# Kernel tuning notes

Measured on AMD Instinct MI355X. Metric: run time of the kernel, lower is better.

The kernel has to match this reference:

```python
import jax, jax.numpy as jnp
import numpy as np
import math

B, CK, CV, O, T, H, W = 2, 64, 512, 2, 16, 30, 54


def setup_inputs() -> dict:
    key = jax.random.key(0)
    k1, k2, k3, k4, k5 = jax.random.split(key, 5)
    return {
        'query_key': jax.random.normal(k1, (B, CK, H, W), jnp.float32),
        'query_selection': jax.random.uniform(k2, (B, CK, H, W), jnp.float32),
        'memory_key': jax.random.normal(k3, (B, CK, T, H, W), jnp.float32),
        'memory_shrinkage': jax.random.uniform(k4, (B, 1, T, H, W), jnp.float32),
        'memory_value': jax.random.normal(k5, (B, O, CV, T, H, W), jnp.float32),
    }


def reference(query_key, query_selection, memory_key, memory_shrinkage, memory_value):
    b, ck, h, w = query_key.shape
    t = memory_key.shape[2]
    n = t * h * w          # memory bank size
    hw = h * w             # query size
    o, cv = memory_value.shape[1], memory_value.shape[2]

    mk = memory_key.reshape(b, ck, n)             # B CK N
    ms = memory_shrinkage.reshape(b, 1, n)        # B 1 N
    qk = query_key.reshape(b, ck, hw)             # B CK HW
    qe = query_selection.reshape(b, ck, hw)       # B CK HW

    # negative squared L2 distance, selection-weighted per channel:
    # -sum_c qe_c * (mk_c - qk_c)^2 = -a_sq + 2ab - b_sq
    a_sq = jnp.einsum('bcn,bcq->bnq', mk * mk, qe)          # B N HW
    two_ab = 2.0 * jnp.einsum('bcn,bcq->bnq', mk, qk * qe)  # B N HW
    b_sq = jnp.sum(qe * qk * qk, axis=1, keepdims=True)     # B 1 HW
    similarity = (-a_sq + two_ab - b_sq)
    # shrinkage scaling + 1/sqrt(CK)
    similarity = similarity * ms.reshape(b, n, 1) * (1.0 / math.sqrt(ck))

    # softmax over the memory axis N
    affinity = jax.nn.softmax(similarity, axis=1)           # B N HW

    # weighted readout
    mv = memory_value.reshape(b, o * cv, n)                 # B (O*CV) N
    mem = jnp.einsum('bvn,bnq->bvq', mv, affinity)          # B (O*CV) HW
    return mem.reshape(b, o, cv, h, w)
```

## Files before the change

kernel.cpp:

```cpp
#include <hip/hip_runtime.h>
#include <stdint.h>

#define CKP 128
#define OCV 1024
#define NTOT 25920
#define HW 1620
#define HWP 1664
#define QT 128
#define VT 256
#define NC 64
#define NQT 13
#define NS 2
#define CHUNKS_TOTAL 405
#define CHUNK_SPLIT 203

typedef _Float16 f16x8 __attribute__((ext_vector_type(8)));
typedef _Float16 f16x4 __attribute__((ext_vector_type(4)));
typedef float f32x4 __attribute__((ext_vector_type(4)));

__device__ __forceinline__ void gload_lds16(const void* g, void* l) {
  __builtin_amdgcn_global_load_lds(
      (const __attribute__((address_space(1))) uint32_t*)g,
      (__attribute__((address_space(3))) uint32_t*)l, 16, 0, 0);
}

__global__ void k_prep_mv(const float* __restrict__ mv, _Float16* __restrict__ mvh) {
  int i = blockIdx.x * 256 + threadIdx.x;
  const float4* s = (const float4*)mv + (size_t)i * 2;
  float4 a = s[0], b = s[1];
  f16x8 o;
  o[0]=(_Float16)a.x; o[1]=(_Float16)a.y; o[2]=(_Float16)a.z; o[3]=(_Float16)a.w;
  o[4]=(_Float16)b.x; o[5]=(_Float16)b.y; o[6]=(_Float16)b.z; o[7]=(_Float16)b.w;
  *((f16x8*)mvh + i) = o;
}

__global__ void k_prep_mk(const float* __restrict__ mk, _Float16* __restrict__ mkp) {
  __shared__ _Float16 LT[64 * CKP];
  int b = blockIdx.y, n0 = blockIdx.x * 64;
  int c4 = threadIdx.x >> 6, nl = threadIdx.x & 63;
  for (int c = c4; c < 64; c += 4) {
    float v = mk[((size_t)(b * 64 + c)) * NTOT + n0 + nl];
    LT[nl * CKP + c]      = (_Float16)v;
    LT[nl * CKP + 64 + c] = (_Float16)(v * v);
  }
  __syncthreads();
  #pragma unroll
  for (int k = 0; k < 4; ++k) {
    int idx = threadIdx.x + 256 * k;
    int n = idx >> 4, c16 = idx & 15;
    *((uint4*)(mkp + ((size_t)b * NTOT + n0 + n) * CKP + c16 * 8)) =
        *((const uint4*)(&LT[n * CKP + c16 * 8]));
  }
}

__global__ void k_prep_q(const float* __restrict__ qk, const float* __restrict__ qe,
                         _Float16* __restrict__ qp, float* __restrict__ bsq) {
  __shared__ _Float16 LT[QT * CKP];
  int b = blockIdx.y, q0 = blockIdx.x * QT;
  int t = threadIdx.x;
  int q = q0 + t;
  bool valid = q < HW;
  float acc = 0.f;
  for (int c = 0; c < 64; ++c) {
    float a = valid ? qk[((size_t)(b * 64 + c)) * HW + q] : 0.f;
    float e = valid ? qe[((size_t)(b * 64 + c)) * HW + q] : 0.f;
    LT[t * CKP + c]      = (_Float16)(2.f * a * e);
    LT[t * CKP + 64 + c] = (_Float16)(-e);
    acc += e * a * a;
  }
  bsq[(size_t)b * HWP + q] = acc;
  __syncthreads();
  #pragma unroll
  for (int k = 0; k < 16; ++k) {
    int idx = t + 128 * k;
    int qq = idx >> 4, c16 = idx & 15;
    *((uint4*)(qp + ((size_t)b * HWP + q0 + qq) * CKP + c16 * 8)) =
        *((const uint4*)(&LT[qq * CKP + c16 * 8]));
  }
}

__launch_bounds__(512, 1)
__global__ void k_main(const _Float16* __restrict__ mvh, const _Float16* __restrict__ mkp,
                       const _Float16* __restrict__ qp, const float* __restrict__ bsq,
                       const float* __restrict__ ms,
                       float* __restrict__ pO, float* __restrict__ lpart) {
  const int wgid = blockIdx.x;
  const int xcd = wgid & 7, kk = wgid >> 3;
  const int gsel = (kk >= NQT) ? 1 : 0;
  const int qt = kk - gsel * NQT;
  const int vt = ((xcd & 1) << 1) | gsel;
  const int bn = xcd >> 1;
  const int b = bn >> 1, nsp = bn & 1;

  const int tid = threadIdx.x;
  const int w = tid >> 6, l = tid & 63;
  const int l15 = l & 15, g = l >> 4;

  __shared__ _Float16 MVs[2][VT * NC];
  __shared__ _Float16 MKs[2][NC * CKP];
  __shared__ _Float16 Ps[2][QT * NC];
  __shared__ float lred[QT * 8];

  const int qw = w & 3, nh = w >> 2;
  const int wv = w & 3, wq = w >> 2;

  const int cBeg = nsp ? CHUNK_SPLIT : 0;
  const int cEnd = nsp ? CHUNKS_TOTAL : CHUNK_SPLIT;

  const char* mvb[4]; int dmv[4];
  #pragma unroll
  for (int k = 0; k < 4; ++k) {
    int idx = k * 512 + tid;
    int v = idx >> 3, s = idx & 7, j = s ^ (v & 7);
    mvb[k] = (const char*)(mvh + ((size_t)b * OCV + vt * VT + v) * NTOT + j * 8);
    dmv[k] = idx * 16;
  }
  const char* mkb[2]; int dmk[2];
  #pragma unroll
  for (int k = 0; k < 2; ++k) {
    int idx = k * 512 + tid;
    int n = idx >> 4, s = idx & 15, j = s ^ (n & 7);
    mkb[k] = (const char*)(mkp + ((size_t)b * NTOT + n) * CKP + j * 8);
    dmk[k] = idx * 16;
  }
  const float* msb = ms + (size_t)b * NTOT + nh * 32 + g * 4;

  f16x8 qreg[2][4];
  float bq[2];
  #pragma unroll
  for (int j = 0; j < 2; ++j) {
    int q_loc = qw * 32 + j * 16 + l15;
    const _Float16* qrow = qp + ((size_t)b * HWP + qt * QT + q_loc) * CKP;
    #pragma unroll
    for (int ks = 0; ks < 4; ++ks) qreg[j][ks] = *((const f16x8*)(qrow + (ks * 4 + g) * 8));
    bq[j] = bsq[(size_t)b * HWP + qt * QT + q_loc];
  }

  f32x4 acc[4][4];
  #pragma unroll
  for (int i = 0; i < 4; ++i)
    #pragma unroll
    for (int j = 0; j < 4; ++j) acc[i][j] = (f32x4)0.f;
  float lp0 = 0.f, lp1 = 0.f;

  auto stage_mv = [&](int ch, int buf) {
    size_t o = (size_t)ch * (NC * 2);
    char* d = (char*)MVs[buf];
    #pragma unroll
    for (int k = 0; k < 4; ++k) gload_lds16(mvb[k] + o, d + dmv[k]);
  };
  auto stage_mk = [&](int ch, int buf) {
    size_t o = (size_t)ch * (NC * CKP * 2);
    char* d = (char*)MKs[buf];
    #pragma unroll
    for (int k = 0; k < 2; ++k) gload_lds16(mkb[k] + o, d + dmk[k]);
  };

  auto do_S = [&](int kb, int pb, float4 mA, float4 mB) {
    const _Float16* MKc = MKs[kb];
    f32x4 sacc[2][2];
    #pragma unroll
    for (int i2 = 0; i2 < 2; ++i2)
      #pragma unroll
      for (int j = 0; j < 2; ++j) sacc[i2][j] = (f32x4)0.f;
    #pragma unroll
    for (int ks = 0; ks < 4; ++ks) {
      f16x8 af[2];
      #pragma unroll
      for (int i2 = 0; i2 < 2; ++i2) {
        int n_loc = nh * 32 + i2 * 16 + l15;
        af[i2] = *((const f16x8*)(&MKc[n_loc * CKP + (((ks * 4 + g) ^ (n_loc & 7)) * 8)]));
      }
      #pragma unroll
      for (int i2 = 0; i2 < 2; ++i2)
        #pragma unroll
        for (int j = 0; j < 2; ++j)
          sacc[i2][j] = __builtin_amdgcn_mfma_f32_16x16x32_f16(af[i2], qreg[j][ks], sacc[i2][j], 0, 0, 0);
    }
    const float K = 0.125f * 1.44269504f;
    #pragma unroll
    for (int i2 = 0; i2 < 2; ++i2) {
      int nbase = nh * 32 + i2 * 16 + g * 4;
      float m0 = (i2 ? mB.x : mA.x) * K;
      float m1 = (i2 ? mB.y : mA.y) * K;
      float m2 = (i2 ? mB.z : mA.z) * K;
      float m3 = (i2 ? mB.w : mA.w) * K;
      #pragma unroll
      for (int j = 0; j < 2; ++j) {
        int q_loc = qw * 32 + j * 16 + l15;
        float bqv = bq[j];
        float p0 = exp2f((sacc[i2][j][0] - bqv) * m0);
        float p1 = exp2f((sacc[i2][j][1] - bqv) * m1);
        float p2 = exp2f((sacc[i2][j][2] - bqv) * m2);
        float p3 = exp2f((sacc[i2][j][3] - bqv) * m3);
        float psum = (p0 + p1) + (p2 + p3);
        if (j == 0) lp0 += psum; else lp1 += psum;
        f16x4 ph;
        ph[0]=(_Float16)p0; ph[1]=(_Float16)p1; ph[2]=(_Float16)p2; ph[3]=(_Float16)p3;
        int nb = nbase >> 3;
        int off4 = nbase & 7;
        *((f16x4*)(&Ps[pb][q_loc * NC + ((nb ^ (q_loc & 7)) * 8) + off4])) = ph;
      }
    }
  };

  auto do_RO = [&](int mb, int pb) {
    const _Float16* MVc = MVs[mb];
    const _Float16* Pc = Ps[pb];
    #pragma unroll
    for (int ks = 0; ks < 2; ++ks) {
      f16x8 av[4], bp[4];
      #pragma unroll
      for (int i = 0; i < 4; ++i) {
        int v_loc = wv * 64 + i * 16 + l15;
        av[i] = *((const f16x8*)(&MVc[v_loc * NC + (((ks * 4 + g) ^ (v_loc & 7)) * 8)]));
      }
      #pragma unroll
      for (int j = 0; j < 4; ++j) {
        int q_loc = wq * 64 + j * 16 + l15;
        bp[j] = *((const f16x8*)(&Pc[q_loc * NC + (((ks * 4 + g) ^ (q_loc & 7)) * 8)]));
      }
      #pragma unroll
      for (int i = 0; i < 4; ++i)
        #pragma unroll
        for (int j = 0; j < 4; ++j)
          acc[i][j] = __builtin_amdgcn_mfma_f32_16x16x32_f16(av[i], bp[j], acc[i][j], 0, 0, 0);
    }
  };

  stage_mv(cBeg, 0);
  stage_mk(cBeg, 0);
  if (cBeg + 1 < cEnd) stage_mk(cBeg + 1, 1);
  float4 mA0 = *(const float4*)(msb + (size_t)cBeg * NC);
  float4 mB0 = *(const float4*)(msb + (size_t)cBeg * NC + 16);
  asm volatile("s_waitcnt vmcnt(0)" ::: "memory");
  __builtin_amdgcn_s_barrier();
  __builtin_amdgcn_sched_barrier(0);
  do_S(0, 0, mA0, mB0);
  asm volatile("s_waitcnt lgkmcnt(0)" ::: "memory");
  __builtin_amdgcn_s_barrier();
  __builtin_amdgcn_sched_barrier(0);

  const int numCh = cEnd - cBeg;
  for (int i = 0; i < numCh; ++i) {
    const int ch = cBeg + i;
    const int cur = i & 1, nxt = cur ^ 1;
    const bool hv = (ch + 1 < cEnd);
    float4 mA, mB;
    if (hv) {
      mA = *(const float4*)(msb + (size_t)(ch + 1) * NC);
      mB = *(const float4*)(msb + (size_t)(ch + 1) * NC + 16);
    }
    __builtin_amdgcn_sched_barrier(0);
    if (hv) stage_mv(ch + 1, nxt);
    if (ch + 2 < cEnd) stage_mk(ch + 2, cur);
    if (hv) do_S(nxt, nxt, mA, mB);
    do_RO(cur, cur);
    asm volatile("s_waitcnt vmcnt(0) lgkmcnt(0)" ::: "memory");
    __builtin_amdgcn_s_barrier();
    __builtin_amdgcn_sched_barrier(0);
  }

  {
    int q0a = qw * 32 + l15;
    lred[q0a * 8 + nh * 4 + g] = lp0;
    lred[(q0a + 16) * 8 + nh * 4 + g] = lp1;
  }
  __syncthreads();
  if (tid < QT) {
    float s = 0.f;
    #pragma unroll
    for (int j = 0; j < 8; ++j) s += lred[tid * 8 + j];
    lpart[((size_t)(b * NS + nsp)) * HWP + qt * QT + tid] = s;
  }
  #pragma unroll
  for (int i = 0; i < 4; ++i) {
    #pragma unroll
    for (int j = 0; j < 4; ++j) {
      #pragma unroll
      for (int r = 0; r < 4; ++r) {
        int v_glob = vt * VT + wv * 64 + i * 16 + g * 4 + r;
        int q_l = qt * QT + wq * 64 + j * 16 + l15;
        pO[(((size_t)(b * NS + nsp)) * OCV + v_glob) * HWP + q_l] = acc[i][j][r];
      }
    }
  }
}

__global__ void k_reduce(const float* __restrict__ pO, const float* __restrict__ lpart,
                         float* __restrict__ out) {
  int i = blockIdx.x * 256 + threadIdx.x;
  int q4 = i % 405;
  int rest = i / 405;
  int v = rest & (OCV - 1);
  int b = rest >> 10;
  int q = q4 * 4;
  float apx = 0.f, apy = 0.f, apz = 0.f, apw = 0.f;
  float alx = 0.f, aly = 0.f, alz = 0.f, alw = 0.f;
  #pragma unroll
  for (int s = 0; s < NS; ++s) {
    const float4 p = *((const float4*)(pO + (((size_t)(b * NS + s)) * OCV + v) * HWP + q));
    const float4 lv = *((const float4*)(lpart + ((size_t)(b * NS + s)) * HWP + q));
    apx += p.x; apy += p.y; apz += p.z; apw += p.w;
    alx += lv.x; aly += lv.y; alz += lv.z; alw += lv.w;
  }
  float4 o;
  o.x = apx / alx; o.y = apy / aly; o.z = apz / alz; o.w = apw / alw;
  *((float4*)(out + ((size_t)b * OCV + v) * HW + q)) = o;
}

extern "C" void kernel_launch(void* const* d_in, const int* in_sizes, int n_in,
                              void* d_out, int out_size, void* d_ws, size_t ws_size,
                              hipStream_t stream) {
  const float* qk = (const float*)d_in[0];
  const float* qe = (const float*)d_in[1];
  const float* mk = (const float*)d_in[2];
  const float* ms = (const float*)d_in[3];
  const float* mv = (const float*)d_in[4];
  float* out = (float*)d_out;

  const size_t sz_mvh = (size_t)2 * OCV * NTOT * 2;
  const size_t sz_mkp = (size_t)2 * NTOT * CKP * 2;
  const size_t sz_qp  = (size_t)2 * HWP * CKP * 2;
  const size_t sz_bsq = (size_t)2 * HWP * 4;
  const size_t need = sz_mvh + sz_mkp + sz_qp + sz_bsq
                    + (size_t)2 * NS * HWP * 4 + (size_t)2 * NS * OCV * HWP * 4;
  if (ws_size < need) return;

  char* p = (char*)d_ws;
  _Float16* mvh = (_Float16*)p; p += sz_mvh;
  _Float16* mkp = (_Float16*)p; p += sz_mkp;
  _Float16* qp  = (_Float16*)p; p += sz_qp;
  float* bsqw   = (float*)p;    p += sz_bsq;
  float* lpart  = (float*)p;    p += (size_t)2 * NS * HWP * 4;
  float* pO     = (float*)p;

  k_prep_mv<<<25920, 256, 0, stream>>>(mv, mvh);
  k_prep_mk<<<dim3(405, 2), 256, 0, stream>>>(mk, mkp);
  k_prep_q<<<dim3(NQT, 2), QT, 0, stream>>>(qk, qe, qp, bsqw);
  k_main<<<8 * 26, 512, 0, stream>>>(mvh, mkp, qp, bsqw, ms, pO, lpart);
  k_reduce<<<3240, 256, 0, stream>>>(pO, lpart, out);
}
```

Before: 561.3 us.

## Halve chunk size, split memory axis four ways and raise occupancy

The memory axis N is now split into four partitions instead of two, and each chunk covers 32 memory columns instead of 64. This doubles the grid to 416 workgroups, and launch bounds now allow up to four blocks per CU, so more workgroups can run at once across the CUs. The LDS swizzles are adjusted to the new chunk width, and s_setprio is wrapped around the MFMA sections. In exchange the partial-output workspace and the final reduction traffic double, and the launch-bounds hint tightens the register budget, which risks spilling the 64-float accumulator tile.

```diff
diff --git a/kernel.cpp b/kernel.cpp
--- a/kernel.cpp
+++ b/kernel.cpp
@@ -8,11 +8,11 @@
 #define HWP 1664
 #define QT 128
 #define VT 256
-#define NC 64
+#define NC 32
 #define NQT 13
-#define NS 2
-#define CHUNKS_TOTAL 405
-#define CHUNK_SPLIT 203
+#define NS 4
+#define CHUNKS_TOTAL 810
+#define CPN 203
 
 typedef _Float16 f16x8 __attribute__((ext_vector_type(8)));
 typedef _Float16 f16x4 __attribute__((ext_vector_type(4)));
@@ -79,18 +79,15 @@
   }
 }
 
-__launch_bounds__(512, 1)
+__launch_bounds__(512, 4)
 __global__ void k_main(const _Float16* __restrict__ mvh, const _Float16* __restrict__ mkp,
                        const _Float16* __restrict__ qp, const float* __restrict__ bsq,
                        const float* __restrict__ ms,
                        float* __restrict__ pO, float* __restrict__ lpart) {
   const int wgid = blockIdx.x;
   const int xcd = wgid & 7, kk = wgid >> 3;
-  const int gsel = (kk >= NQT) ? 1 : 0;
-  const int qt = kk - gsel * NQT;
-  const int vt = ((xcd & 1) << 1) | gsel;
-  const int bn = xcd >> 1;
-  const int b = bn >> 1, nsp = bn & 1;
+  const int b = xcd >> 2, nsp = xcd & 3;
+  const int vt = kk / NQT, qt = kk % NQT;
 
   const int tid = threadIdx.x;
   const int w = tid >> 6, l = tid & 63;
@@ -104,26 +101,26 @@
   const int qw = w & 3, nh = w >> 2;
   const int wv = w & 3, wq = w >> 2;
 
-  const int cBeg = nsp ? CHUNK_SPLIT : 0;
-  const int cEnd = nsp ? CHUNKS_TOTAL : CHUNK_SPLIT;
-
-  const char* mvb[4]; int dmv[4];
-  #pragma unroll
-  for (int k = 0; k < 4; ++k) {
+  const int cBeg = nsp * CPN;
+  int ce = cBeg + CPN; if (ce > CHUNKS_TOTAL) ce = CHUNKS_TOTAL;
+  const int cEnd = ce;
+
+  const char* mvb[2]; int dmv[2];
+  #pragma unroll
+  for (int k = 0; k < 2; ++k) {
     int idx = k * 512 + tid;
-    int v = idx >> 3, s = idx & 7, j = s ^ (v & 7);
+    int v = idx >> 2, s = idx & 3, j = s ^ ((v >> 1) & 3);
     mvb[k] = (const char*)(mvh + ((size_t)b * OCV + vt * VT + v) * NTOT + j * 8);
     dmv[k] = idx * 16;
   }
-  const char* mkb[2]; int dmk[2];
-  #pragma unroll
-  for (int k = 0; k < 2; ++k) {
-    int idx = k * 512 + tid;
+  const char* mkb; int dmk;
+  {
+    int idx = tid;
     int n = idx >> 4, s = idx & 15, j = s ^ (n & 7);
-    mkb[k] = (const char*)(mkp + ((size_t)b * NTOT + n) * CKP + j * 8);
-    dmk[k] = idx * 16;
-  }
-  const float* msb = ms + (size_t)b * NTOT + nh * 32 + g * 4;
+    mkb = (const char*)(mkp + ((size_t)b * NTOT + n) * CKP + j * 8);
+    dmk = idx * 16;
+  }
+  const float* msb = ms + (size_t)b * NTOT + nh * 16 + g * 4;
 
   f16x8 qreg[2][4];
   float bq[2];
@@ -147,96 +144,80 @@
     size_t o = (size_t)ch * (NC * 2);
     char* d = (char*)MVs[buf];
     #pragma unroll
-    for (int k = 0; k < 4; ++k) gload_lds16(mvb[k] + o, d + dmv[k]);
+    for (int k = 0; k < 2; ++k) gload_lds16(mvb[k] + o, d + dmv[k]);
   };
   auto stage_mk = [&](int ch, int buf) {
     size_t o = (size_t)ch * (NC * CKP * 2);
-    char* d = (char*)MKs[buf];
-    #pragma unroll
-    for (int k = 0; k < 2; ++k) gload_lds16(mkb[k] + o, d + dmk[k]);
+    gload_lds16(mkb + o, (char*)MKs[buf] + dmk);
   };
 
-  auto do_S = [&](int kb, int pb, float4 mA, float4 mB) {
+  auto do_S = [&](int kb, int pb, float4 mA) {
     const _Float16* MKc = MKs[kb];
-    f32x4 sacc[2][2];
-    #pragma unroll
-    for (int i2 = 0; i2 < 2; ++i2)
+    f32x4 sacc[2];
+    sacc[0] = (f32x4)0.f; sacc[1] = (f32x4)0.f;
+    const int n_loc = nh * 16 + l15;
+    __builtin_amdgcn_s_setprio(1);
+    #pragma unroll
+    for (int ks = 0; ks < 4; ++ks) {
+      f16x8 af = *((const f16x8*)(&MKc[n_loc * CKP + (((ks * 4 + g) ^ (n_loc & 7)) * 8)]));
       #pragma unroll
-      for (int j = 0; j < 2; ++j) sacc[i2][j] = (f32x4)0.f;
-    #pragma unroll
-    for (int ks = 0; ks < 4; ++ks) {
-      f16x8 af[2];
-      #pragma unroll
-      for (int i2 = 0; i2 < 2; ++i2) {
-        int n_loc = nh * 32 + i2 * 16 + l15;
-        af[i2] = *((const f16x8*)(&MKc[n_loc * CKP + (((ks * 4 + g) ^ (n_loc & 7)) * 8)]));
-      }
-      #pragma unroll
-      for (int i2 = 0; i2 < 2; ++i2)
-        #pragma unroll
-        for (int j = 0; j < 2; ++j)
-          sacc[i2][j] = __builtin_amdgcn_mfma_f32_16x16x32_f16(af[i2], qreg[j][ks], sacc[i2][j], 0, 0, 0);
-    }
+      for (int j = 0; j < 2; ++j)
+        sacc[j] = __builtin_amdgcn_mfma_f32_16x16x32_f16(af, qreg[j][ks], sacc[j], 0, 0, 0);
+    }
+    __builtin_amdgcn_s_setprio(0);
     const float K = 0.125f * 1.44269504f;
-    #pragma unroll
-    for (int i2 = 0; i2 < 2; ++i2) {
-      int nbase = nh * 32 + i2 * 16 + g * 4;
-      float m0 = (i2 ? mB.x : mA.x) * K;
-      float m1 = (i2 ? mB.y : mA.y) * K;
-      float m2 = (i2 ? mB.z : mA.z) * K;
-      float m3 = (i2 ? mB.w : mA.w) * K;
-      #pragma unroll
-      for (int j = 0; j < 2; ++j) {
-        int q_loc = qw * 32 + j * 16 + l15;
-        float bqv = bq[j];
-        float p0 = exp2f((sacc[i2][j][0] - bqv) * m0);
-        float p1 = exp2f((sacc[i2][j][1] - bqv) * m1);
-        float p2 = exp2f((sacc[i2][j][2] - bqv) * m2);
-        float p3 = exp2f((sacc[i2][j][3] - bqv) * m3);
-        float psum = (p0 + p1) + (p2 + p3);
-        if (j == 0) lp0 += psum; else lp1 += psum;
-        f16x4 ph;
-        ph[0]=(_Float16)p0; ph[1]=(_Float16)p1; ph[2]=(_Float16)p2; ph[3]=(_Float16)p3;
-        int nb = nbase >> 3;
-        int off4 = nbase & 7;
-        *((f16x4*)(&Ps[pb][q_loc * NC + ((nb ^ (q_loc & 7)) * 8) + off4])) = ph;
-      }
+    const int nbase = nh * 16 + g * 4;
+    float m0 = mA.x * K, m1 = mA.y * K, m2 = mA.z * K, m3 = mA.w * K;
+    #pragma unroll
+    for (int j = 0; j < 2; ++j) {
+      int q_loc = qw * 32 + j * 16 + l15;
+      float bqv = bq[j];
+      float p0 = exp2f((sacc[j][0] - bqv) * m0);
+      float p1 = exp2f((sacc[j][1] - bqv) * m1);
+      float p2 = exp2f((sacc[j][2] - bqv) * m2);
+      float p3 = exp2f((sacc[j][3] - bqv) * m3);
+      float psum = (p0 + p1) + (p2 + p3);
+      if (j == 0) lp0 += psum; else lp1 += psum;
+      f16x4 ph;
+      ph[0]=(_Float16)p0; ph[1]=(_Float16)p1; ph[2]=(_Float16)p2; ph[3]=(_Float16)p3;
+      int nb = nbase >> 3;
+      int off4 = nbase & 7;
+      int slot = nb ^ ((q_loc >> 1) & 3);
+      *((f16x4*)(&Ps[pb][q_loc * NC + slot * 8 + off4])) = ph;
     }
   };
 
   auto do_RO = [&](int mb, int pb) {
     const _Float16* MVc = MVs[mb];
     const _Float16* Pc = Ps[pb];
-    #pragma unroll
-    for (int ks = 0; ks < 2; ++ks) {
-      f16x8 av[4], bp[4];
+    f16x8 av[4], bp[4];
+    #pragma unroll
+    for (int i = 0; i < 4; ++i) {
+      int v_loc = wv * 64 + i * 16 + l15;
+      av[i] = *((const f16x8*)(&MVc[v_loc * NC + ((g ^ ((v_loc >> 1) & 3)) * 8)]));
+    }
+    #pragma unroll
+    for (int j = 0; j < 4; ++j) {
+      int q_loc = wq * 64 + j * 16 + l15;
+      bp[j] = *((const f16x8*)(&Pc[q_loc * NC + ((g ^ ((q_loc >> 1) & 3)) * 8)]));
+    }
+    __builtin_amdgcn_s_setprio(1);
+    #pragma unroll
+    for (int i = 0; i < 4; ++i)
       #pragma unroll
-      for (int i = 0; i < 4; ++i) {
-        int v_loc = wv * 64 + i * 16 + l15;
-        av[i] = *((const f16x8*)(&MVc[v_loc * NC + (((ks * 4 + g) ^ (v_loc & 7)) * 8)]));
-      }
-      #pragma unroll
-      for (int j = 0; j < 4; ++j) {
-        int q_loc = wq * 64 + j * 16 + l15;
-        bp[j] = *((const f16x8*)(&Pc[q_loc * NC + (((ks * 4 + g) ^ (q_loc & 7)) * 8)]));
-      }
-      #pragma unroll
-      for (int i = 0; i < 4; ++i)
-        #pragma unroll
-        for (int j = 0; j < 4; ++j)
-          acc[i][j] = __builtin_amdgcn_mfma_f32_16x16x32_f16(av[i], bp[j], acc[i][j], 0, 0, 0);
-    }
+      for (int j = 0; j < 4; ++j)
+        acc[i][j] = __builtin_amdgcn_mfma_f32_16x16x32_f16(av[i], bp[j], acc[i][j], 0, 0, 0);
+    __builtin_amdgcn_s_setprio(0);
   };
 
   stage_mv(cBeg, 0);
   stage_mk(cBeg, 0);
   if (cBeg + 1 < cEnd) stage_mk(cBeg + 1, 1);
   float4 mA0 = *(const float4*)(msb + (size_t)cBeg * NC);
-  float4 mB0 = *(const float4*)(msb + (size_t)cBeg * NC + 16);
   asm volatile("s_waitcnt vmcnt(0)" ::: "memory");
   __builtin_amdgcn_s_barrier();
   __builtin_amdgcn_sched_barrier(0);
-  do_S(0, 0, mA0, mB0);
+  do_S(0, 0, mA0);
   asm volatile("s_waitcnt lgkmcnt(0)" ::: "memory");
   __builtin_amdgcn_s_barrier();
   __builtin_amdgcn_sched_barrier(0);
@@ -246,15 +227,12 @@
     const int ch = cBeg + i;
     const int cur = i & 1, nxt = cur ^ 1;
     const bool hv = (ch + 1 < cEnd);
-    float4 mA, mB;
-    if (hv) {
-      mA = *(const float4*)(msb + (size_t)(ch + 1) * NC);
-      mB = *(const float4*)(msb + (size_t)(ch + 1) * NC + 16);
-    }
+    float4 mA;
+    if (hv) mA = *(const float4*)(msb + (size_t)(ch + 1) * NC);
     __builtin_amdgcn_sched_barrier(0);
     if (hv) stage_mv(ch + 1, nxt);
     if (ch + 2 < cEnd) stage_mk(ch + 2, cur);
-    if (hv) do_S(nxt, nxt, mA, mB);
+    if (hv) do_S(nxt, nxt, mA);
     do_RO(cur, cur);
     asm volatile("s_waitcnt vmcnt(0) lgkmcnt(0)" ::: "memory");
     __builtin_amdgcn_s_barrier();
@@ -338,6 +316,6 @@
   k_prep_mv<<<25920, 256, 0, stream>>>(mv, mvh);
   k_prep_mk<<<dim3(405, 2), 256, 0, stream>>>(mk, mkp);
   k_prep_q<<<dim3(NQT, 2), QT, 0, stream>>>(qk, qe, qp, bsqw);
-  k_main<<<8 * 26, 512, 0, stream>>>(mvh, mkp, qp, bsqw, ms, pO, lpart);
+  k_main<<<8 * 52, 512, 0, stream>>>(mvh, mkp, qp, bsqw, ms, pO, lpart);
   k_reduce<<<3240, 256, 0, stream>>>(pO, lpart, out);
 }
```

Measured after the change: 1.027 ms. 1.83x slower.

## Triple-buffer memory values and serialize score/readout phases with single P buffer

Applied to the files above, without the earlier changes.

Moves memory-value staging to a three-deep LDS ring and prefetches two chunks ahead, using partial vmcnt waits instead of draining all loads each iteration. The probability tile drops to a single buffer, so the score step now runs after the readout behind an extra barrier instead of overlapping with it. The lred scratch reuses the key buffer to save LDS. The goal is to hide global-load latency better, at the cost of two barriers per chunk and less overlap between the exp/MFMA phases.

```diff
diff --git a/kernel.cpp b/kernel.cpp
--- a/kernel.cpp
+++ b/kernel.cpp
@@ -96,16 +96,16 @@
   const int w = tid >> 6, l = tid & 63;
   const int l15 = l & 15, g = l >> 4;
 
-  __shared__ _Float16 MVs[2][VT * NC];
+  __shared__ _Float16 MVs[3][VT * NC];
   __shared__ _Float16 MKs[2][NC * CKP];
-  __shared__ _Float16 Ps[2][QT * NC];
-  __shared__ float lred[QT * 8];
+  __shared__ _Float16 Ps[QT * NC];
 
   const int qw = w & 3, nh = w >> 2;
   const int wv = w & 3, wq = w >> 2;
 
   const int cBeg = nsp ? CHUNK_SPLIT : 0;
   const int cEnd = nsp ? CHUNKS_TOTAL : CHUNK_SPLIT;
+  const int numCh = cEnd - cBeg;
 
   const char* mvb[4]; int dmv[4];
   #pragma unroll
@@ -156,7 +156,7 @@
     for (int k = 0; k < 2; ++k) gload_lds16(mkb[k] + o, d + dmk[k]);
   };
 
-  auto do_S = [&](int kb, int pb, float4 mA, float4 mB) {
+  auto do_S = [&](int kb, float4 mA, float4 mB) {
     const _Float16* MKc = MKs[kb];
     f32x4 sacc[2][2];
     #pragma unroll
@@ -199,14 +199,13 @@
         ph[0]=(_Float16)p0; ph[1]=(_Float16)p1; ph[2]=(_Float16)p2; ph[3]=(_Float16)p3;
         int nb = nbase >> 3;
         int off4 = nbase & 7;
-        *((f16x4*)(&Ps[pb][q_loc * NC + ((nb ^ (q_loc & 7)) * 8) + off4])) = ph;
+        *((f16x4*)(&Ps[q_loc * NC + ((nb ^ (q_loc & 7)) * 8) + off4])) = ph;
       }
     }
   };
 
-  auto do_RO = [&](int mb, int pb) {
+  auto do_RO = [&](int mb) {
     const _Float16* MVc = MVs[mb];
-    const _Float16* Pc = Ps[pb];
     #pragma unroll
     for (int ks = 0; ks < 2; ++ks) {
       f16x8 av[4], bp[4];
@@ -218,7 +217,7 @@
       #pragma unroll
       for (int j = 0; j < 4; ++j) {
         int q_loc = wq * 64 + j * 16 + l15;
-        bp[j] = *((const f16x8*)(&Pc[q_loc * NC + (((ks * 4 + g) ^ (q_loc & 7)) * 8)]));
+        bp[j] = *((const f16x8*)(&Ps[q_loc * NC + (((ks * 4 + g) ^ (q_loc & 7)) * 8)]));
       }
       #pragma unroll
       for (int i = 0; i < 4; ++i)
@@ -228,39 +227,50 @@
     }
   };
 
+  stage_mk(cBeg, 0);
   stage_mv(cBeg, 0);
-  stage_mk(cBeg, 0);
-  if (cBeg + 1 < cEnd) stage_mk(cBeg + 1, 1);
-  float4 mA0 = *(const float4*)(msb + (size_t)cBeg * NC);
-  float4 mB0 = *(const float4*)(msb + (size_t)cBeg * NC + 16);
-  asm volatile("s_waitcnt vmcnt(0)" ::: "memory");
+  stage_mk(cBeg + 1, 1);
+  stage_mv(cBeg + 1, 1);
+  float4 msP0 = *(const float4*)(msb + (size_t)cBeg * NC);
+  float4 msP1 = *(const float4*)(msb + (size_t)cBeg * NC + 16);
+  float4 msA  = *(const float4*)(msb + (size_t)(cBeg + 1) * NC);
+  float4 msAh = *(const float4*)(msb + (size_t)(cBeg + 1) * NC + 16);
+  float4 msB  = *(const float4*)(msb + (size_t)(cBeg + 2) * NC);
+  float4 msBh = *(const float4*)(msb + (size_t)(cBeg + 2) * NC + 16);
+  asm volatile("s_waitcnt vmcnt(0) lgkmcnt(0)" ::: "memory");
   __builtin_amdgcn_s_barrier();
   __builtin_amdgcn_sched_barrier(0);
-  do_S(0, 0, mA0, mB0);
+  do_S(0, msP0, msP1);
   asm volatile("s_waitcnt lgkmcnt(0)" ::: "memory");
   __builtin_amdgcn_s_barrier();
   __builtin_amdgcn_sched_barrier(0);
 
-  const int numCh = cEnd - cBeg;
+  int r0 = 0;
   for (int i = 0; i < numCh; ++i) {
     const int ch = cBeg + i;
-    const int cur = i & 1, nxt = cur ^ 1;
-    const bool hv = (ch + 1 < cEnd);
-    float4 mA, mB;
-    if (hv) {
-      mA = *(const float4*)(msb + (size_t)(ch + 1) * NC);
-      mB = *(const float4*)(msb + (size_t)(ch + 1) * NC + 16);
-    }
-    __builtin_amdgcn_sched_barrier(0);
-    if (hv) stage_mv(ch + 1, nxt);
-    if (ch + 2 < cEnd) stage_mk(ch + 2, cur);
-    if (hv) do_S(nxt, nxt, mA, mB);
-    do_RO(cur, cur);
-    asm volatile("s_waitcnt vmcnt(0) lgkmcnt(0)" ::: "memory");
+    int r2 = r0 + 2; if (r2 >= 3) r2 -= 3;
+    float4 msN = msB, msNh = msBh;
+    if (i + 4 <= numCh) {
+      msN  = *(const float4*)(msb + (size_t)(ch + 3) * NC);
+      msNh = *(const float4*)(msb + (size_t)(ch + 3) * NC + 16);
+    }
+    if (i + 2 < numCh) {
+      stage_mk(ch + 2, i & 1);
+      stage_mv(ch + 2, r2);
+    }
+    do_RO(r0);
+    asm volatile("s_waitcnt vmcnt(11) lgkmcnt(0)" ::: "memory");
     __builtin_amdgcn_s_barrier();
     __builtin_amdgcn_sched_barrier(0);
-  }
-
+    if (i + 1 < numCh) do_S((i + 1) & 1, msA, msAh);
+    msA = msB; msAh = msBh; msB = msN; msBh = msNh;
+    asm volatile("s_waitcnt vmcnt(7) lgkmcnt(0)" ::: "memory");
+    __builtin_amdgcn_s_barrier();
+    __builtin_amdgcn_sched_barrier(0);
+    r0 = (r0 + 1 == 3) ? 0 : r0 + 1;
+  }
+
+  float* lred = (float*)(&MKs[0][0]);
   {
     int q0a = qw * 32 + l15;
     lred[q0a * 8 + nh * 4 + g] = lp0;
```

After: 546.5 us. 2.6% less time.
